# Kernel tuning notes

Measured on AMD Instinct MI355X. Metric: run time of the kernel, lower is better.

The kernel has to match this reference:

```python
import jax, jax.numpy as jnp
import numpy as np

BLOCK = 256
H, D = 16, 128          # num_attention_heads, head_dim
HID = 2048              # hidden_size (= H*D)
FFN = 2048              # intermediate_size
E, TOPK = 8, 2          # num_local_experts, num_experts_per_tok
EPS_LN = 1e-5           # rms_norm_eps for layer norms
EPS_ATTN = float(np.finfo(np.float32).eps)  # torch RMSNorm default eps


def rmsnorm(x, w, eps):
    v = jnp.mean(jnp.square(x), axis=-1, keepdims=True)
    return x * jax.lax.rsqrt(v + eps) * w


def lightning_attn(x, slope, qkv_w, gate_w, norm_w, out_w):
    # x: [B,N,HID]; slope: [H,1,1]
    B, N, _ = x.shape
    qkv = jax.nn.silu(x @ qkv_w.T).reshape(B, N, H, 3 * D)
    q, k, v = jnp.split(qkv, 3, axis=-1)
    q = q.transpose(0, 2, 1, 3)  # [B,H,N,D]
    k = k.transpose(0, 2, 1, 3)
    v = v.transpose(0, 2, 1, 3)

    NB = N // BLOCK
    ar = jnp.arange(BLOCK, dtype=jnp.float32) + 1.0
    q_decay = jnp.exp(-slope * ar[:, None])             # [H,BLOCK,1]
    k_decay = jnp.exp(-slope * (BLOCK - ar[:, None]))   # [H,BLOCK,1]
    idx = ar[:, None] - ar[None, :]                      # [BLOCK,BLOCK]
    diag_decay = jnp.exp(jnp.where(idx >= 0, -(slope * idx), -jnp.inf))  # [H,BLOCK,BLOCK]
    block_decay = jnp.exp(-slope * BLOCK)                # [H,1,1]

    qb = q.reshape(B, H, NB, BLOCK, D).transpose(2, 0, 1, 3, 4)  # [NB,B,H,BLOCK,D]
    kb = k.reshape(B, H, NB, BLOCK, D).transpose(2, 0, 1, 3, 4)
    vb = v.reshape(B, H, NB, BLOCK, D).transpose(2, 0, 1, 3, 4)

    def step(kv, blk):
        qi, ki, vi = blk                                   # [B,H,BLOCK,D]
        o_nd = jnp.einsum('bhmd,bhde->bhme', qi * q_decay, kv)
        qk = jnp.einsum('bhmd,bhnd->bhmn', qi, ki) * diag_decay[None]
        o_d = jnp.einsum('bhmn,bhne->bhme', qk, vi)
        kv = block_decay * kv + jnp.einsum('bhmd,bhme->bhde', ki * k_decay, vi)
        return kv, o_nd + o_d

    kv0 = jnp.zeros((B, H, D, D), jnp.float32)
    _, out = jax.lax.scan(step, kv0, (qb, kb, vb))         # out: [NB,B,H,BLOCK,D]
    out = out.transpose(1, 2, 0, 3, 4).reshape(B, H, N, D)
    out = out.transpose(0, 2, 1, 3).reshape(B, N, H * D)   # b h n d -> b n (h d)
    out = rmsnorm(out, norm_w, EPS_ATTN)
    out = jax.nn.sigmoid(x @ gate_w.T) * out
    return out @ out_w.T


def moe(x, router_w, w1, w2, w3):
    # x: [B,N,HID]
    B, N, _ = x.shape
    xt = x.reshape(B * N, HID)                             # [T,HID]
    T = B * N
    logits = xt @ router_w.T                               # [T,E]
    probs = jax.nn.softmax(logits.astype(jnp.float32), axis=-1)
    w, sel = jax.lax.top_k(probs, TOPK)                    # [T,TOPK]
    w = w / jnp.sum(w, axis=-1, keepdims=True)
    w = w.astype(xt.dtype)
    # dense combine weights [T,E] (top-k experts are distinct)
    cw = jnp.zeros((T, E), xt.dtype).at[jnp.arange(T)[:, None], sel].add(w)
    h1 = jax.nn.silu(jnp.einsum('td,efd->tef', xt, w1))    # [T,E,FFN]
    h3 = jnp.einsum('td,efd->tef', xt, w3)
    ye = jnp.einsum('tef,edf->ted', h1 * h3, w2)           # [T,E,HID]
    out = jnp.einsum('te,ted->td', cw, ye)
    return out.reshape(B, N, HID)


def setup_inputs() -> dict:
    key = jax.random.key(0)
    ks = jax.random.split(key, 12)
    s = 0.02
    B, N = 1, 1024
    x = jax.random.normal(ks[0], (B, N, HID), jnp.float32)
    # ALiBi-like positive per-head decay rates
    slope_rate = (1.0 / (2.0 ** (8.0 * (jnp.arange(H, dtype=jnp.float32) + 1) / H))).reshape(H, 1, 1)
    return {
        'x': x,
        'slope_rate': slope_rate,
        'ln1_w': jnp.ones((HID,), jnp.float32),
        'ln2_w': jnp.ones((HID,), jnp.float32),
        'qkv_w': jax.random.normal(ks[1], (3 * H * D, HID), jnp.float32) * s,
        'ogate_w': jax.random.normal(ks[2], (H * D, HID), jnp.float32) * s,
        'anorm_w': jnp.ones((H * D,), jnp.float32),
        'aout_w': jax.random.normal(ks[3], (HID, H * D), jnp.float32) * s,
        'router_w': jax.random.normal(ks[4], (E, HID), jnp.float32) * s,
        'w1': jax.random.normal(ks[5], (E, FFN, HID), jnp.float32) * s,
        'w2': jax.random.normal(ks[6], (E, HID, FFN), jnp.float32) * s,
        'w3': jax.random.normal(ks[7], (E, FFN, HID), jnp.float32) * s,
    }


def reference(x, slope_rate, ln1_w, ln2_w, qkv_w, ogate_w, anorm_w, aout_w, router_w, w1, w2, w3):
    # pre-norm residual decoder layer (alpha=beta=1, postnorm=False, no shared MoE)
    r = x
    h = rmsnorm(x, ln1_w, EPS_LN)
    h = r + lightning_attn(h, slope_rate, qkv_w, ogate_w, anorm_w, aout_w)
    r = h
    h2 = rmsnorm(h, ln2_w, EPS_LN)
    return r + moe(h2, router_w, w1, w2, w3)
```

## Files before the change

kernel.cpp:

```cpp
#include <hip/hip_runtime.h>
#include <math.h>

#define NTOK 1024
#define NHID 2048
#define NQKV 6144
#define NHEADS 16
#define DHEAD 128
#define ABLK 256
#define NEXPERT 8
#define NFFN 2048
#define EPS_LN 1e-5f
#define EPS_ATTN 1.1920929e-7f

typedef __bf16 bf8v __attribute__((ext_vector_type(8)));
typedef __bf16 bf4v __attribute__((ext_vector_type(4)));
typedef float f4v __attribute__((ext_vector_type(4)));

static __device__ __forceinline__ f4v mfma16(bf8v a, bf8v b, f4v c) {
  return __builtin_amdgcn_mfma_f32_16x16x32_bf16(a, b, c, 0, 0, 0);
}

static __device__ __forceinline__ void gl2lds16(const float* g, float* l) {
  __builtin_amdgcn_global_load_lds(
      (const __attribute__((address_space(1))) float*)g,
      (__attribute__((address_space(3))) float*)l, 16, 0, 0);
}

__global__ __launch_bounds__(256) void rms_kernel(const float* __restrict__ in,
                                                  const float* __restrict__ w,
                                                  float* __restrict__ out,
                                                  const float* __restrict__ gate,
                                                  float* __restrict__ copy_out,
                                                  float eps) {
  const int row = blockIdx.x, tid = threadIdx.x;
  const float* p = in + (size_t)row * NHID;
  float4 v0 = *(const float4*)(p + 4 * tid);
  float4 v1 = *(const float4*)(p + 1024 + 4 * tid);
  float ss = v0.x * v0.x + v0.y * v0.y + v0.z * v0.z + v0.w * v0.w
           + v1.x * v1.x + v1.y * v1.y + v1.z * v1.z + v1.w * v1.w;
  for (int off = 32; off > 0; off >>= 1) ss += __shfl_down(ss, off);
  __shared__ float red[4];
  const int wv = tid >> 6, ln = tid & 63;
  if (ln == 0) red[wv] = ss;
  __syncthreads();
  const float tot = red[0] + red[1] + red[2] + red[3];
  const float rinv = rsqrtf(tot * (1.f / NHID) + eps);
  float4 w0 = *(const float4*)(w + 4 * tid);
  float4 w1 = *(const float4*)(w + 1024 + 4 * tid);
  float4 o0, o1;
  o0.x = v0.x * rinv * w0.x; o0.y = v0.y * rinv * w0.y;
  o0.z = v0.z * rinv * w0.z; o0.w = v0.w * rinv * w0.w;
  o1.x = v1.x * rinv * w1.x; o1.y = v1.y * rinv * w1.y;
  o1.z = v1.z * rinv * w1.z; o1.w = v1.w * rinv * w1.w;
  if (gate) {
    const float* gp = gate + (size_t)row * NHID;
    float4 g0 = *(const float4*)(gp + 4 * tid);
    float4 g1 = *(const float4*)(gp + 1024 + 4 * tid);
    o0.x *= g0.x; o0.y *= g0.y; o0.z *= g0.z; o0.w *= g0.w;
    o1.x *= g1.x; o1.y *= g1.y; o1.z *= g1.z; o1.w *= g1.w;
  }
  *(float4*)(out + (size_t)row * NHID + 4 * tid) = o0;
  *(float4*)(out + (size_t)row * NHID + 1024 + 4 * tid) = o1;
  if (copy_out) {
    *(float4*)(copy_out + (size_t)row * NHID + 4 * tid) = v0;
    *(float4*)(copy_out + (size_t)row * NHID + 1024 + 4 * tid) = v1;
  }
}

enum { GM_QKV = 0, GM_GATE = 1, GM_AOUT = 2, GM_MOE1 = 3, GM_MOE3 = 4, GM_MOE2 = 5 };

struct GArgs {
  const float* A; const float* B; float* C;
  const float* res;
  float* q_s; float* k_s; float* v_s;
  const int* perm; const int* segoff; const float* pw;
  float* outp;
  int N, K;
};

template <int MODE>
__global__ __launch_bounds__(256, 3) void gemm_bt(GArgs g) {
  const int n0 = blockIdx.x * 64;
  const int m0 = blockIdx.y * 128;
  int segbase = 0, cnt = 0x40000000, e = 0;
  if constexpr (MODE >= GM_MOE1) {
    e = blockIdx.z;
    segbase = g.segoff[e];
    cnt = g.segoff[e + 1] - segbase;
    if (m0 >= cnt) return;
  }
  const float* Bp = g.B + (size_t)e * g.N * g.K + (size_t)n0 * g.K;
  __shared__ float As[2][128 * 32];
  __shared__ float Bs[2][64 * 32];
  const int tid = threadIdx.x;
  const int w = tid >> 6, lane = tid & 63;
  const int wm = (w >> 1) * 64, wn = (w & 1) * 32;
  const int lm = lane & 15, quad = lane >> 4;
  const int lr = lane >> 3;
  const int coff = ((lane & 7) ^ lr) * 4;
  const int K = g.K;

  const float* aptr[4];
  const float* bptr[2];
#pragma unroll
  for (int qi = 0; qi < 4; qi++) {
    const int r = (w * 4 + qi) * 8 + lr;
    const int m = m0 + r;
    long grow;
    if constexpr (MODE == GM_MOE1 || MODE == GM_MOE3) {
      int mm = m < cnt ? m : cnt - 1;
      grow = g.perm[segbase + mm];
    } else if constexpr (MODE == GM_MOE2) {
      grow = segbase + (m < cnt ? m : cnt - 1);
    } else {
      grow = m;
    }
    aptr[qi] = g.A + (size_t)grow * K + coff;
  }
#pragma unroll
  for (int qi = 0; qi < 2; qi++) {
    const int r = (w * 2 + qi) * 8 + lr;
    bptr[qi] = Bp + (size_t)r * K + coff;
  }

  const f4v fz = {0.f, 0.f, 0.f, 0.f};
  f4v acc[4][2];
#pragma unroll
  for (int i = 0; i < 4; i++) {
    acc[i][0] = fz; acc[i][1] = fz;
  }

  const int KT = K >> 5;
#pragma unroll
  for (int qi = 0; qi < 4; qi++) gl2lds16(aptr[qi], &As[0][(w * 4 + qi) * 256]);
#pragma unroll
  for (int qi = 0; qi < 2; qi++) gl2lds16(bptr[qi], &Bs[0][(w * 2 + qi) * 256]);
  asm volatile("s_waitcnt vmcnt(0)" ::: "memory");
  __builtin_amdgcn_s_barrier();

  for (int t = 0; t < KT; ++t) {
    const int cur = t & 1;
    if (t + 1 < KT) {
      const int k1 = (t + 1) << 5;
#pragma unroll
      for (int qi = 0; qi < 4; qi++)
        gl2lds16(aptr[qi] + k1, &As[cur ^ 1][(w * 4 + qi) * 256]);
#pragma unroll
      for (int qi = 0; qi < 2; qi++)
        gl2lds16(bptr[qi] + k1, &Bs[cur ^ 1][(w * 2 + qi) * 256]);
    }
    bf8v af[4], bfv[2];
    const int sw = lm & 7;
#pragma unroll
    for (int i = 0; i < 4; i++) {
      const int ra = wm + i * 16 + lm;
      const float4 x0 = *(const float4*)&As[cur][ra * 32 + (((quad * 2) ^ sw) << 2)];
      const float4 x1 = *(const float4*)&As[cur][ra * 32 + (((quad * 2 + 1) ^ sw) << 2)];
      bf8v t8;
      t8[0] = (__bf16)x0.x; t8[1] = (__bf16)x0.y; t8[2] = (__bf16)x0.z; t8[3] = (__bf16)x0.w;
      t8[4] = (__bf16)x1.x; t8[5] = (__bf16)x1.y; t8[6] = (__bf16)x1.z; t8[7] = (__bf16)x1.w;
      af[i] = t8;
    }
#pragma unroll
    for (int j = 0; j < 2; j++) {
      const int rb = wn + j * 16 + lm;
      const float4 x0 = *(const float4*)&Bs[cur][rb * 32 + (((quad * 2) ^ sw) << 2)];
      const float4 x1 = *(const float4*)&Bs[cur][rb * 32 + (((quad * 2 + 1) ^ sw) << 2)];
      bf8v t8;
      t8[0] = (__bf16)x0.x; t8[1] = (__bf16)x0.y; t8[2] = (__bf16)x0.z; t8[3] = (__bf16)x0.w;
      t8[4] = (__bf16)x1.x; t8[5] = (__bf16)x1.y; t8[6] = (__bf16)x1.z; t8[7] = (__bf16)x1.w;
      bfv[j] = t8;
    }
#pragma unroll
    for (int i = 0; i < 4; i++)
#pragma unroll
      for (int j = 0; j < 2; j++) acc[i][j] = mfma16(af[i], bfv[j], acc[i][j]);
    asm volatile("s_waitcnt vmcnt(0) lgkmcnt(0)" ::: "memory");
    __builtin_amdgcn_s_barrier();
  }

#pragma unroll
  for (int i = 0; i < 4; i++) {
#pragma unroll
    for (int r = 0; r < 4; r++) {
      const int m = m0 + wm + i * 16 + quad * 4 + r;
      int tok = 0;
      float wgt = 0.f;
      if constexpr (MODE == GM_MOE2) {
        if (m < cnt) { tok = g.perm[segbase + m]; wgt = g.pw[segbase + m]; }
      }
#pragma unroll
      for (int j = 0; j < 2; j++) {
        const int col = n0 + wn + j * 16 + lm;
        float v = acc[i][j][r];
        if constexpr (MODE == GM_QKV) {
          v = v / (1.f + expf(-v));
          int head = col / 384;
          int rem = col - head * 384;
          int which = rem >> 7;
          int d = rem & 127;
          float* dst = which == 0 ? g.q_s : (which == 1 ? g.k_s : g.v_s);
          dst[((size_t)head * NTOK + m) * DHEAD + d] = v;
        } else if constexpr (MODE == GM_GATE) {
          g.C[(size_t)m * g.N + col] = 1.f / (1.f + expf(-v));
        } else if constexpr (MODE == GM_AOUT) {
          g.C[(size_t)m * g.N + col] = v + g.res[(size_t)m * g.N + col];
        } else if constexpr (MODE == GM_MOE1) {
          if (m < cnt) g.C[(size_t)(segbase + m) * g.N + col] = v / (1.f + expf(-v));
        } else if constexpr (MODE == GM_MOE3) {
          if (m < cnt) {
            size_t ix = (size_t)(segbase + m) * g.N + col;
            g.C[ix] = v * g.res[ix];
          }
        } else if constexpr (MODE == GM_MOE2) {
          if (m < cnt) atomicAdd(&g.outp[(size_t)tok * NHID + col], wgt * v);
        }
      }
    }
  }
}

__global__ __launch_bounds__(512) void attn_pass1(const float* __restrict__ k_s,
                                                  const float* __restrict__ v_s,
                                                  const float* __restrict__ slope,
                                                  float* __restrict__ S) {
  const int h = blockIdx.x >> 2, b = blockIdx.x & 3;
  const float s = slope[h];
  __shared__ __bf16 kT[128][40] __attribute__((aligned(16)));
  __shared__ __bf16 vT[128][40] __attribute__((aligned(16)));
  const int tid = threadIdx.x, wave = tid >> 6, lane = tid & 63;
  const int lm = lane & 15, quad = lane >> 4;
  const float* kb = k_s + ((size_t)h * NTOK + b * ABLK) * DHEAD;
  const float* vb = v_s + ((size_t)h * NTOK + b * ABLK) * DHEAD;
  const int sd = tid & 127, sg = (tid >> 7) * 8;
  const f4v fz = {0.f, 0.f, 0.f, 0.f};
  f4v acc[8];
#pragma unroll
  for (int j = 0; j < 8; j++) acc[j] = fz;
  for (int ic = 0; ic < 8; ic++) {
    __syncthreads();
    bf8v kq, vq;
#pragma unroll
    for (int ii = 0; ii < 8; ii++) {
      int ig = ic * 32 + sg + ii;
      float kd = expf(-s * (float)(ABLK - 1 - ig));
      kq[ii] = (__bf16)(kb[(size_t)ig * DHEAD + sd] * kd);
      vq[ii] = (__bf16)(vb[(size_t)ig * DHEAD + sd]);
    }
    *(bf8v*)&kT[sd][sg] = kq;
    *(bf8v*)&vT[sd][sg] = vq;
    __syncthreads();
    bf8v a = *(const bf8v*)&kT[wave * 16 + lm][quad * 8];
#pragma unroll
    for (int j = 0; j < 8; j++) {
      bf8v bb = *(const bf8v*)&vT[j * 16 + lm][quad * 8];
      acc[j] = mfma16(a, bb, acc[j]);
    }
  }
  float* Sp = S + (size_t)(h * 4 + b) * (128 * 128);
#pragma unroll
  for (int j = 0; j < 8; j++)
#pragma unroll
    for (int r = 0; r < 4; r++)
      Sp[(size_t)(wave * 16 + quad * 4 + r) * 128 + j * 16 + lm] = acc[j][r];
}

__global__ __launch_bounds__(512) void attn_pass2(const float* __restrict__ q_s,
                                                  const float* __restrict__ k_s,
                                                  const float* __restrict__ v_s,
                                                  const float* __restrict__ slope,
                                                  const float* __restrict__ S,
                                                  float* __restrict__ attn_raw) {
  const int h = blockIdx.x >> 2, b = blockIdx.x & 3;
  const float s = slope[h];
  __shared__ __bf16 kvb[128][136] __attribute__((aligned(16)));
  __shared__ __bf16 vT[128][40] __attribute__((aligned(16)));
  __shared__ __bf16 ki[32][136] __attribute__((aligned(16)));
  __shared__ __bf16 qkb[256][40] __attribute__((aligned(16)));
  const int tid = threadIdx.x, w = tid >> 6, lane = tid & 63;
  const int lm = lane & 15, quad = lane >> 4;
  {
    const int sd = tid >> 2;
    const int e0 = (tid & 3) * 32;
    float vals[32];
#pragma unroll
    for (int u = 0; u < 32; u++) vals[u] = 0.f;
    for (int j = 0; j < b; j++) {
      float c = expf(-s * 256.f * (float)(b - 1 - j));
      const float* Sp = S + (size_t)(h * 4 + j) * (128 * 128) + (size_t)sd * 128 + e0;
#pragma unroll
      for (int u4 = 0; u4 < 8; u4++) {
        float4 sv = *(const float4*)(Sp + u4 * 4);
        vals[u4 * 4 + 0] += c * sv.x; vals[u4 * 4 + 1] += c * sv.y;
        vals[u4 * 4 + 2] += c * sv.z; vals[u4 * 4 + 3] += c * sv.w;
      }
    }
#pragma unroll
    for (int u = 0; u < 32; u++) kvb[e0 + u][sd] = (__bf16)vals[u];
  }
  __syncthreads();
  const float* qb = q_s + ((size_t)h * NTOK + b * ABLK) * DHEAD;
  const float* kb = k_s + ((size_t)h * NTOK + b * ABLK) * DHEAD;
  const float* vb = v_s + ((size_t)h * NTOK + b * ABLK) * DHEAD;
  bf8v aq[2][4];
#pragma unroll
  for (int mf = 0; mf < 2; mf++) {
    const int m = w * 32 + mf * 16 + lm;
#pragma unroll
    for (int kc = 0; kc < 4; kc++) {
      const float* pp = qb + (size_t)m * DHEAD + kc * 32 + quad * 8;
      float4 u0 = *(const float4*)pp;
      float4 u1 = *(const float4*)(pp + 4);
      bf8v t;
      t[0] = (__bf16)u0.x; t[1] = (__bf16)u0.y; t[2] = (__bf16)u0.z; t[3] = (__bf16)u0.w;
      t[4] = (__bf16)u1.x; t[5] = (__bf16)u1.y; t[6] = (__bf16)u1.z; t[7] = (__bf16)u1.w;
      aq[mf][kc] = t;
    }
  }
  const f4v fz = {0.f, 0.f, 0.f, 0.f};
  f4v accO[2][8];
#pragma unroll
  for (int mf = 0; mf < 2; mf++)
#pragma unroll
    for (int nf = 0; nf < 8; nf++) accO[mf][nf] = fz;
#pragma unroll
  for (int kc = 0; kc < 4; kc++) {
#pragma unroll
    for (int nf = 0; nf < 8; nf++) {
      bf8v bb = *(const bf8v*)&kvb[nf * 16 + lm][kc * 32 + quad * 8];
      accO[0][nf] = mfma16(aq[0][kc], bb, accO[0][nf]);
      accO[1][nf] = mfma16(aq[1][kc], bb, accO[1][nf]);
    }
  }
#pragma unroll
  for (int mf = 0; mf < 2; mf++) {
#pragma unroll
    for (int r = 0; r < 4; r++) {
      const int m = w * 32 + mf * 16 + quad * 4 + r;
      const float qd = expf(-s * (float)(m + 1));
#pragma unroll
      for (int nf = 0; nf < 8; nf++) accO[mf][nf][r] *= qd;
    }
  }
  for (int ic = 0; ic < 8; ic++) {
    __syncthreads();
    {
      const int si = tid >> 4, dc = (tid & 15) * 8;
      const float* pp = kb + (size_t)(ic * 32 + si) * DHEAD + dc;
      float4 u0 = *(const float4*)pp;
      float4 u1 = *(const float4*)(pp + 4);
      bf8v t;
      t[0] = (__bf16)u0.x; t[1] = (__bf16)u0.y; t[2] = (__bf16)u0.z; t[3] = (__bf16)u0.w;
      t[4] = (__bf16)u1.x; t[5] = (__bf16)u1.y; t[6] = (__bf16)u1.z; t[7] = (__bf16)u1.w;
      *(bf8v*)&ki[si][dc] = t;
    }
    {
      const int se = tid & 127, sg = (tid >> 7) * 8;
      bf8v t;
#pragma unroll
      for (int ii = 0; ii < 8; ii++)
        t[ii] = (__bf16)vb[(size_t)(ic * 32 + sg + ii) * DHEAD + se];
      *(bf8v*)&vT[se][sg] = t;
    }
    __syncthreads();
    f4v acc2[2][2];
    acc2[0][0] = fz; acc2[0][1] = fz; acc2[1][0] = fz; acc2[1][1] = fz;
#pragma unroll
    for (int kc = 0; kc < 4; kc++) {
#pragma unroll
      for (int f = 0; f < 2; f++) {
        bf8v bk = *(const bf8v*)&ki[f * 16 + lm][kc * 32 + quad * 8];
        acc2[0][f] = mfma16(aq[0][kc], bk, acc2[0][f]);
        acc2[1][f] = mfma16(aq[1][kc], bk, acc2[1][f]);
      }
    }
#pragma unroll
    for (int mf = 0; mf < 2; mf++) {
#pragma unroll
      for (int f = 0; f < 2; f++) {
#pragma unroll
        for (int r = 0; r < 4; r++) {
          const int m = w * 32 + mf * 16 + quad * 4 + r;
          const int i = ic * 32 + f * 16 + lm;
          float v = acc2[mf][f][r];
          v = (m >= i) ? v * expf(-s * (float)(m - i)) : 0.f;
          qkb[m][f * 16 + lm] = (__bf16)v;
        }
      }
    }
    __syncthreads();
#pragma unroll
    for (int mf = 0; mf < 2; mf++) {
      bf8v aqk = *(const bf8v*)&qkb[w * 32 + mf * 16 + lm][quad * 8];
#pragma unroll
      for (int nf = 0; nf < 8; nf++) {
        bf8v bv = *(const bf8v*)&vT[nf * 16 + lm][quad * 8];
        accO[mf][nf] = mfma16(aqk, bv, accO[mf][nf]);
      }
    }
  }
  float* op = attn_raw + (size_t)(b * ABLK) * NHID + h * DHEAD;
#pragma unroll
  for (int mf = 0; mf < 2; mf++)
#pragma unroll
    for (int r = 0; r < 4; r++) {
      const int m = w * 32 + mf * 16 + quad * 4 + r;
#pragma unroll
      for (int nf = 0; nf < 8; nf++)
        op[(size_t)m * NHID + nf * 16 + lm] = accO[mf][nf][r];
    }
}

__global__ __launch_bounds__(256) void router_kernel(const float* __restrict__ h2,
                                                     const float* __restrict__ rw,
                                                     int* __restrict__ eidx,
                                                     float* __restrict__ ew) {
  const int wave = threadIdx.x >> 6, lane = threadIdx.x & 63;
  const int t = blockIdx.x * 4 + wave;
  float a[8];
#pragma unroll
  for (int e = 0; e < 8; e++) a[e] = 0.f;
  for (int d = lane; d < NHID; d += 64) {
    float xv = h2[(size_t)t * NHID + d];
#pragma unroll
    for (int e = 0; e < 8; e++) a[e] += xv * rw[(size_t)e * NHID + d];
  }
#pragma unroll
  for (int e = 0; e < 8; e++)
    for (int off = 32; off > 0; off >>= 1) a[e] += __shfl_down(a[e], off);
  if (lane == 0) {
    int i1 = 0;
#pragma unroll
    for (int e = 1; e < 8; e++)
      if (a[e] > a[i1]) i1 = e;
    int i2 = i1 == 0 ? 1 : 0;
#pragma unroll
    for (int e = 0; e < 8; e++) {
      if (e == i1 || e == i2) continue;
      if (a[e] > a[i2]) i2 = e;
    }
    float be = expf(a[i2] - a[i1]);
    float w1 = 1.f / (1.f + be), w2 = be / (1.f + be);
    eidx[2 * t] = i1; eidx[2 * t + 1] = i2;
    ew[2 * t] = w1; ew[2 * t + 1] = w2;
  }
}

__global__ __launch_bounds__(256) void build_lists(const int* __restrict__ eidx,
                                                   const float* __restrict__ ew,
                                                   int* __restrict__ segoff,
                                                   int* __restrict__ perm,
                                                   float* __restrict__ pw) {
  __shared__ int cnt[8], cur[8], offs[9];
  const int tid = threadIdx.x;
  if (tid < 8) cnt[tid] = 0;
  __syncthreads();
  for (int t = tid; t < NTOK; t += 256) {
    atomicAdd(&cnt[eidx[2 * t]], 1);
    atomicAdd(&cnt[eidx[2 * t + 1]], 1);
  }
  __syncthreads();
  if (tid == 0) {
    int o = 0;
    for (int e = 0; e < 8; e++) { offs[e] = o; o += cnt[e]; }
    offs[8] = o;
    for (int e = 0; e < 9; e++) segoff[e] = offs[e];
  }
  __syncthreads();
  if (tid < 8) cur[tid] = offs[tid];
  __syncthreads();
  for (int t = tid; t < NTOK; t += 256) {
    for (int k = 0; k < 2; k++) {
      int e = eidx[2 * t + k];
      int pos = atomicAdd(&cur[e], 1);
      perm[pos] = t;
      pw[pos] = ew[2 * t + k];
    }
  }
}

extern "C" void kernel_launch(void* const* d_in, const int* in_sizes, int n_in,
                              void* d_out, int out_size, void* d_ws, size_t ws_size,
                              hipStream_t stream) {
  (void)in_sizes; (void)n_in; (void)out_size; (void)ws_size;
  const float* x        = (const float*)d_in[0];
  const float* slope    = (const float*)d_in[1];
  const float* ln1_w    = (const float*)d_in[2];
  const float* ln2_w    = (const float*)d_in[3];
  const float* qkv_w    = (const float*)d_in[4];
  const float* ogate_w  = (const float*)d_in[5];
  const float* anorm_w  = (const float*)d_in[6];
  const float* aout_w   = (const float*)d_in[7];
  const float* router_w = (const float*)d_in[8];
  const float* w1       = (const float*)d_in[9];
  const float* w2       = (const float*)d_in[10];
  const float* w3       = (const float*)d_in[11];
  float* out = (float*)d_out;
  float* ws  = (float*)d_ws;

  const size_t MW = (size_t)NTOK * NHID;
  float* a_ln     = ws;
  float* q_s      = ws + MW;
  float* k_s      = ws + 2 * MW;
  float* v_s      = ws + 3 * MW;
  float* Sbuf     = ws + 4 * MW;
  float* attn_raw = ws + 4 * MW + MW / 2;
  float* gatebuf  = ws + 5 * MW + MW / 2;
  float* t1       = ws + 4 * MW + MW / 2;
  float* rbase    = ws + 6 * MW + MW / 2;
  int*   eidx   = (int*)rbase;
  float* ew     = rbase + 2048;
  int*   segoff = (int*)(rbase + 4096);
  int*   perm   = (int*)(rbase + 4112);
  float* pw     = rbase + 6160;
  float* h_res = k_s;
  float* h2    = v_s;
  float* ag    = a_ln;

  rms_kernel<<<dim3(NTOK), dim3(256), 0, stream>>>(x, ln1_w, a_ln, nullptr, nullptr, EPS_LN);
  {
    GArgs g{}; g.A = a_ln; g.B = qkv_w; g.q_s = q_s; g.k_s = k_s; g.v_s = v_s;
    g.N = NQKV; g.K = NHID;
    gemm_bt<GM_QKV><<<dim3(NQKV / 64, NTOK / 128), dim3(256), 0, stream>>>(g);
  }
  attn_pass1<<<dim3(64), dim3(512), 0, stream>>>(k_s, v_s, slope, Sbuf);
  attn_pass2<<<dim3(64), dim3(512), 0, stream>>>(q_s, k_s, v_s, slope, Sbuf, attn_raw);
  {
    GArgs g{}; g.A = a_ln; g.B = ogate_w; g.C = gatebuf; g.N = NHID; g.K = NHID;
    gemm_bt<GM_GATE><<<dim3(32, 8), dim3(256), 0, stream>>>(g);
  }
  rms_kernel<<<dim3(NTOK), dim3(256), 0, stream>>>(attn_raw, anorm_w, ag, gatebuf, nullptr, EPS_ATTN);
  {
    GArgs g{}; g.A = ag; g.B = aout_w; g.C = h_res; g.res = x; g.N = NHID; g.K = NHID;
    gemm_bt<GM_AOUT><<<dim3(32, 8), dim3(256), 0, stream>>>(g);
  }
  rms_kernel<<<dim3(NTOK), dim3(256), 0, stream>>>(h_res, ln2_w, h2, nullptr, out, EPS_LN);
  router_kernel<<<dim3(NTOK / 4), dim3(256), 0, stream>>>(h2, router_w, eidx, ew);
  build_lists<<<dim3(1), dim3(256), 0, stream>>>(eidx, ew, segoff, perm, pw);
  {
    GArgs g{}; g.A = h2; g.B = w1; g.C = t1; g.perm = perm; g.segoff = segoff;
    g.N = NFFN; g.K = NHID;
    gemm_bt<GM_MOE1><<<dim3(32, 16, 8), dim3(256), 0, stream>>>(g);
  }
  {
    GArgs g{}; g.A = h2; g.B = w3; g.C = t1; g.res = t1; g.perm = perm; g.segoff = segoff;
    g.N = NFFN; g.K = NHID;
    gemm_bt<GM_MOE3><<<dim3(32, 16, 8), dim3(256), 0, stream>>>(g);
  }
  {
    GArgs g{}; g.A = t1; g.B = w2; g.outp = out; g.perm = perm; g.segoff = segoff; g.pw = pw;
    g.N = NHID; g.K = NFFN;
    gemm_bt<GM_MOE2><<<dim3(32, 16, 8), dim3(256), 0, stream>>>(g);
  }
}
```

Before: 874.8 us.

## Store activations in bf16 and triple-buffer GEMM LDS staging

RMSNorm outputs, the q/k/v buffers and the MoE intermediate are now written in bf16 instead of fp32. This halves activation traffic and lets the GEMM A-tile and the attention kernels load bf16 directly, with no per-tile conversion. The GEMM main loop moves from a double-buffered to a three-stage LDS pipeline with partial vmcnt waits, so loads run two tiles ahead. The cost is extra rounding of activations and intermediates (t1 is rounded twice) and more shared memory per block, which may reduce occupancy.

```diff
diff --git a/kernel.cpp b/kernel.cpp
--- a/kernel.cpp
+++ b/kernel.cpp
@@ -20,17 +20,18 @@
   return __builtin_amdgcn_mfma_f32_16x16x32_bf16(a, b, c, 0, 0, 0);
 }
 
-static __device__ __forceinline__ void gl2lds16(const float* g, float* l) {
+static __device__ __forceinline__ void gl2lds16(const void* g, void* l) {
   __builtin_amdgcn_global_load_lds(
-      (const __attribute__((address_space(1))) float*)g,
-      (__attribute__((address_space(3))) float*)l, 16, 0, 0);
+      (const __attribute__((address_space(1))) unsigned int*)g,
+      (__attribute__((address_space(3))) unsigned int*)l, 16, 0, 0);
 }
 
 __global__ __launch_bounds__(256) void rms_kernel(const float* __restrict__ in,
                                                   const float* __restrict__ w,
-                                                  float* __restrict__ out,
+                                                  __bf16* __restrict__ out_bf,
                                                   const float* __restrict__ gate,
                                                   float* __restrict__ copy_out,
+                                                  float* __restrict__ out_f32,
                                                   float eps) {
   const int row = blockIdx.x, tid = threadIdx.x;
   const float* p = in + (size_t)row * NHID;
@@ -59,8 +60,15 @@
     o0.x *= g0.x; o0.y *= g0.y; o0.z *= g0.z; o0.w *= g0.w;
     o1.x *= g1.x; o1.y *= g1.y; o1.z *= g1.z; o1.w *= g1.w;
   }
-  *(float4*)(out + (size_t)row * NHID + 4 * tid) = o0;
-  *(float4*)(out + (size_t)row * NHID + 1024 + 4 * tid) = o1;
+  bf4v b0, b1;
+  b0[0] = (__bf16)o0.x; b0[1] = (__bf16)o0.y; b0[2] = (__bf16)o0.z; b0[3] = (__bf16)o0.w;
+  b1[0] = (__bf16)o1.x; b1[1] = (__bf16)o1.y; b1[2] = (__bf16)o1.z; b1[3] = (__bf16)o1.w;
+  *(bf4v*)(out_bf + (size_t)row * NHID + 4 * tid) = b0;
+  *(bf4v*)(out_bf + (size_t)row * NHID + 1024 + 4 * tid) = b1;
+  if (out_f32) {
+    *(float4*)(out_f32 + (size_t)row * NHID + 4 * tid) = o0;
+    *(float4*)(out_f32 + (size_t)row * NHID + 1024 + 4 * tid) = o1;
+  }
   if (copy_out) {
     *(float4*)(copy_out + (size_t)row * NHID + 4 * tid) = v0;
     *(float4*)(copy_out + (size_t)row * NHID + 1024 + 4 * tid) = v1;
@@ -70,9 +78,9 @@
 enum { GM_QKV = 0, GM_GATE = 1, GM_AOUT = 2, GM_MOE1 = 3, GM_MOE3 = 4, GM_MOE2 = 5 };
 
 struct GArgs {
-  const float* A; const float* B; float* C;
+  const __bf16* A; const float* B; void* C;
   const float* res;
-  float* q_s; float* k_s; float* v_s;
+  __bf16* q_s; __bf16* k_s; __bf16* v_s;
   const int* perm; const int* segoff; const float* pw;
   float* outp;
   int N, K;
@@ -90,21 +98,18 @@
     if (m0 >= cnt) return;
   }
   const float* Bp = g.B + (size_t)e * g.N * g.K + (size_t)n0 * g.K;
-  __shared__ float As[2][128 * 32];
-  __shared__ float Bs[2][64 * 32];
+  __shared__ __bf16 As[3][128 * 32] __attribute__((aligned(16)));
+  __shared__ float Bs[3][64 * 32] __attribute__((aligned(16)));
   const int tid = threadIdx.x;
   const int w = tid >> 6, lane = tid & 63;
   const int wm = (w >> 1) * 64, wn = (w & 1) * 32;
   const int lm = lane & 15, quad = lane >> 4;
-  const int lr = lane >> 3;
-  const int coff = ((lane & 7) ^ lr) * 4;
   const int K = g.K;
 
-  const float* aptr[4];
-  const float* bptr[2];
-#pragma unroll
-  for (int qi = 0; qi < 4; qi++) {
-    const int r = (w * 4 + qi) * 8 + lr;
+  const __bf16* aptr[2];
+#pragma unroll
+  for (int qi = 0; qi < 2; qi++) {
+    const int r = w * 32 + qi * 16 + (lane >> 2);
     const int m = m0 + r;
     long grow;
     if constexpr (MODE == GM_MOE1 || MODE == GM_MOE3) {
@@ -115,12 +120,18 @@
     } else {
       grow = m;
     }
-    aptr[qi] = g.A + (size_t)grow * K + coff;
-  }
-#pragma unroll
-  for (int qi = 0; qi < 2; qi++) {
-    const int r = (w * 2 + qi) * 8 + lr;
-    bptr[qi] = Bp + (size_t)r * K + coff;
+    const int gc = (lane & 3) ^ (r & 3);
+    aptr[qi] = g.A + (size_t)grow * K + gc * 8;
+  }
+  const float* bptr[2];
+  {
+    const int lr = lane >> 3;
+    const int coff = ((lane & 7) ^ lr) * 4;
+#pragma unroll
+    for (int qi = 0; qi < 2; qi++) {
+      const int r = (w * 2 + qi) * 8 + lr;
+      bptr[qi] = Bp + (size_t)r * K + coff;
+    }
   }
 
   const f4v fz = {0.f, 0.f, 0.f, 0.f};
@@ -131,41 +142,44 @@
   }
 
   const int KT = K >> 5;
-#pragma unroll
-  for (int qi = 0; qi < 4; qi++) gl2lds16(aptr[qi], &As[0][(w * 4 + qi) * 256]);
-#pragma unroll
-  for (int qi = 0; qi < 2; qi++) gl2lds16(bptr[qi], &Bs[0][(w * 2 + qi) * 256]);
-  asm volatile("s_waitcnt vmcnt(0)" ::: "memory");
-  __builtin_amdgcn_s_barrier();
-
+
+#define STAGE(tt, bb)                                      \
+  do {                                                     \
+    const int kk_ = (tt) << 5;                             \
+    gl2lds16(aptr[0] + kk_, &As[bb][(w * 32) * 32]);       \
+    gl2lds16(aptr[1] + kk_, &As[bb][(w * 32 + 16) * 32]);  \
+    gl2lds16(bptr[0] + kk_, &Bs[bb][(w * 16) * 32]);       \
+    gl2lds16(bptr[1] + kk_, &Bs[bb][(w * 16 + 8) * 32]);   \
+  } while (0)
+
+  STAGE(0, 0);
+  STAGE(1, 1);
+
+  const int swa = lm & 3;
+  const int swb = lm & 7;
   for (int t = 0; t < KT; ++t) {
-    const int cur = t & 1;
+    const int cur = t % 3;
     if (t + 1 < KT) {
-      const int k1 = (t + 1) << 5;
-#pragma unroll
-      for (int qi = 0; qi < 4; qi++)
-        gl2lds16(aptr[qi] + k1, &As[cur ^ 1][(w * 4 + qi) * 256]);
-#pragma unroll
-      for (int qi = 0; qi < 2; qi++)
-        gl2lds16(bptr[qi] + k1, &Bs[cur ^ 1][(w * 2 + qi) * 256]);
+      asm volatile("s_waitcnt vmcnt(4)" ::: "memory");
+    } else {
+      asm volatile("s_waitcnt vmcnt(0)" ::: "memory");
+    }
+    __builtin_amdgcn_s_barrier();
+    if (t + 2 < KT) {
+      const int nb = (t + 2) % 3;
+      STAGE(t + 2, nb);
     }
     bf8v af[4], bfv[2];
-    const int sw = lm & 7;
 #pragma unroll
     for (int i = 0; i < 4; i++) {
       const int ra = wm + i * 16 + lm;
-      const float4 x0 = *(const float4*)&As[cur][ra * 32 + (((quad * 2) ^ sw) << 2)];
-      const float4 x1 = *(const float4*)&As[cur][ra * 32 + (((quad * 2 + 1) ^ sw) << 2)];
-      bf8v t8;
-      t8[0] = (__bf16)x0.x; t8[1] = (__bf16)x0.y; t8[2] = (__bf16)x0.z; t8[3] = (__bf16)x0.w;
-      t8[4] = (__bf16)x1.x; t8[5] = (__bf16)x1.y; t8[6] = (__bf16)x1.z; t8[7] = (__bf16)x1.w;
-      af[i] = t8;
+      af[i] = *(const bf8v*)&As[cur][ra * 32 + ((quad ^ swa) << 3)];
     }
 #pragma unroll
     for (int j = 0; j < 2; j++) {
       const int rb = wn + j * 16 + lm;
-      const float4 x0 = *(const float4*)&Bs[cur][rb * 32 + (((quad * 2) ^ sw) << 2)];
-      const float4 x1 = *(const float4*)&Bs[cur][rb * 32 + (((quad * 2 + 1) ^ sw) << 2)];
+      const float4 x0 = *(const float4*)&Bs[cur][rb * 32 + (((quad * 2) ^ swb) << 2)];
+      const float4 x1 = *(const float4*)&Bs[cur][rb * 32 + (((quad * 2 + 1) ^ swb) << 2)];
       bf8v t8;
       t8[0] = (__bf16)x0.x; t8[1] = (__bf16)x0.y; t8[2] = (__bf16)x0.z; t8[3] = (__bf16)x0.w;
       t8[4] = (__bf16)x1.x; t8[5] = (__bf16)x1.y; t8[6] = (__bf16)x1.z; t8[7] = (__bf16)x1.w;
@@ -175,9 +189,8 @@
     for (int i = 0; i < 4; i++)
 #pragma unroll
       for (int j = 0; j < 2; j++) acc[i][j] = mfma16(af[i], bfv[j], acc[i][j]);
-    asm volatile("s_waitcnt vmcnt(0) lgkmcnt(0)" ::: "memory");
-    __builtin_amdgcn_s_barrier();
-  }
+  }
+#undef STAGE
 
 #pragma unroll
   for (int i = 0; i < 4; i++) {
@@ -199,18 +212,20 @@
           int rem = col - head * 384;
           int which = rem >> 7;
           int d = rem & 127;
-          float* dst = which == 0 ? g.q_s : (which == 1 ? g.k_s : g.v_s);
-          dst[((size_t)head * NTOK + m) * DHEAD + d] = v;
+          __bf16* dst = which == 0 ? g.q_s : (which == 1 ? g.k_s : g.v_s);
+          dst[((size_t)head * NTOK + m) * DHEAD + d] = (__bf16)v;
         } else if constexpr (MODE == GM_GATE) {
-          g.C[(size_t)m * g.N + col] = 1.f / (1.f + expf(-v));
+          ((float*)g.C)[(size_t)m * g.N + col] = 1.f / (1.f + expf(-v));
         } else if constexpr (MODE == GM_AOUT) {
-          g.C[(size_t)m * g.N + col] = v + g.res[(size_t)m * g.N + col];
+          ((float*)g.C)[(size_t)m * g.N + col] = v + g.res[(size_t)m * g.N + col];
         } else if constexpr (MODE == GM_MOE1) {
-          if (m < cnt) g.C[(size_t)(segbase + m) * g.N + col] = v / (1.f + expf(-v));
+          if (m < cnt)
+            ((__bf16*)g.C)[(size_t)(segbase + m) * g.N + col] = (__bf16)(v / (1.f + expf(-v)));
         } else if constexpr (MODE == GM_MOE3) {
           if (m < cnt) {
             size_t ix = (size_t)(segbase + m) * g.N + col;
-            g.C[ix] = v * g.res[ix];
+            __bf16* tc = (__bf16*)g.C;
+            tc[ix] = (__bf16)(v * (float)tc[ix]);
           }
         } else if constexpr (MODE == GM_MOE2) {
           if (m < cnt) atomicAdd(&g.outp[(size_t)tok * NHID + col], wgt * v);
@@ -220,8 +235,8 @@
   }
 }
 
-__global__ __launch_bounds__(512) void attn_pass1(const float* __restrict__ k_s,
-                                                  const float* __restrict__ v_s,
+__global__ __launch_bounds__(512) void attn_pass1(const __bf16* __restrict__ k_s,
+                                                  const __bf16* __restrict__ v_s,
                                                   const float* __restrict__ slope,
                                                   float* __restrict__ S) {
   const int h = blockIdx.x >> 2, b = blockIdx.x & 3;
@@ -230,8 +245,8 @@
   __shared__ __bf16 vT[128][40] __attribute__((aligned(16)));
   const int tid = threadIdx.x, wave = tid >> 6, lane = tid & 63;
   const int lm = lane & 15, quad = lane >> 4;
-  const float* kb = k_s + ((size_t)h * NTOK + b * ABLK) * DHEAD;
-  const float* vb = v_s + ((size_t)h * NTOK + b * ABLK) * DHEAD;
+  const __bf16* kb = k_s + ((size_t)h * NTOK + b * ABLK) * DHEAD;
+  const __bf16* vb = v_s + ((size_t)h * NTOK + b * ABLK) * DHEAD;
   const int sd = tid & 127, sg = (tid >> 7) * 8;
   const f4v fz = {0.f, 0.f, 0.f, 0.f};
   f4v acc[8];
@@ -244,8 +259,8 @@
     for (int ii = 0; ii < 8; ii++) {
       int ig = ic * 32 + sg + ii;
       float kd = expf(-s * (float)(ABLK - 1 - ig));
-      kq[ii] = (__bf16)(kb[(size_t)ig * DHEAD + sd] * kd);
-      vq[ii] = (__bf16)(vb[(size_t)ig * DHEAD + sd]);
+      kq[ii] = (__bf16)((float)kb[(size_t)ig * DHEAD + sd] * kd);
+      vq[ii] = vb[(size_t)ig * DHEAD + sd];
     }
     *(bf8v*)&kT[sd][sg] = kq;
     *(bf8v*)&vT[sd][sg] = vq;
@@ -265,9 +280,9 @@
       Sp[(size_t)(wave * 16 + quad * 4 + r) * 128 + j * 16 + lm] = acc[j][r];
 }
 
-__global__ __launch_bounds__(512) void attn_pass2(const float* __restrict__ q_s,
-                                                  const float* __restrict__ k_s,
-                                                  const float* __restrict__ v_s,
+__global__ __launch_bounds__(512) void attn_pass2(const __bf16* __restrict__ q_s,
+                                                  const __bf16* __restrict__ k_s,
+                                                  const __bf16* __restrict__ v_s,
                                                   const float* __restrict__ slope,
                                                   const float* __restrict__ S,
                                                   float* __restrict__ attn_raw) {
@@ -299,23 +314,16 @@
     for (int u = 0; u < 32; u++) kvb[e0 + u][sd] = (__bf16)vals[u];
   }
   __syncthreads();
-  const float* qb = q_s + ((size_t)h * NTOK + b * ABLK) * DHEAD;
-  const float* kb = k_s + ((size_t)h * NTOK + b * ABLK) * DHEAD;
-  const float* vb = v_s + ((size_t)h * NTOK + b * ABLK) * DHEAD;
+  const __bf16* qb = q_s + ((size_t)h * NTOK + b * ABLK) * DHEAD;
+  const __bf16* kb = k_s + ((size_t)h * NTOK + b * ABLK) * DHEAD;
+  const __bf16* vb = v_s + ((size_t)h * NTOK + b * ABLK) * DHEAD;
   bf8v aq[2][4];
 #pragma unroll
   for (int mf = 0; mf < 2; mf++) {
     const int m = w * 32 + mf * 16 + lm;
 #pragma unroll
-    for (int kc = 0; kc < 4; kc++) {
-      const float* pp = qb + (size_t)m * DHEAD + kc * 32 + quad * 8;
-      float4 u0 = *(const float4*)pp;
-      float4 u1 = *(const float4*)(pp + 4);
-      bf8v t;
-      t[0] = (__bf16)u0.x; t[1] = (__bf16)u0.y; t[2] = (__bf16)u0.z; t[3] = (__bf16)u0.w;
-      t[4] = (__bf16)u1.x; t[5] = (__bf16)u1.y; t[6] = (__bf16)u1.z; t[7] = (__bf16)u1.w;
-      aq[mf][kc] = t;
-    }
+    for (int kc = 0; kc < 4; kc++)
+      aq[mf][kc] = *(const bf8v*)(qb + (size_t)m * DHEAD + kc * 32 + quad * 8);
   }
   const f4v fz = {0.f, 0.f, 0.f, 0.f};
   f4v accO[2][8];
@@ -346,20 +354,14 @@
     __syncthreads();
     {
       const int si = tid >> 4, dc = (tid & 15) * 8;
-      const float* pp = kb + (size_t)(ic * 32 + si) * DHEAD + dc;
-      float4 u0 = *(const float4*)pp;
-      float4 u1 = *(const float4*)(pp + 4);
-      bf8v t;
-      t[0] = (__bf16)u0.x; t[1] = (__bf16)u0.y; t[2] = (__bf16)u0.z; t[3] = (__bf16)u0.w;
-      t[4] = (__bf16)u1.x; t[5] = (__bf16)u1.y; t[6] = (__bf16)u1.z; t[7] = (__bf16)u1.w;
-      *(bf8v*)&ki[si][dc] = t;
+      *(bf8v*)&ki[si][dc] = *(const bf8v*)(kb + (size_t)(ic * 32 + si) * DHEAD + dc);
     }
     {
       const int se = tid & 127, sg = (tid >> 7) * 8;
       bf8v t;
 #pragma unroll
       for (int ii = 0; ii < 8; ii++)
-        t[ii] = (__bf16)vb[(size_t)(ic * 32 + sg + ii) * DHEAD + se];
+        t[ii] = vb[(size_t)(ic * 32 + sg + ii) * DHEAD + se];
       *(bf8v*)&vT[se][sg] = t;
     }
     __syncthreads();
@@ -499,25 +501,26 @@
   float* ws  = (float*)d_ws;
 
   const size_t MW = (size_t)NTOK * NHID;
-  float* a_ln     = ws;
-  float* q_s      = ws + MW;
-  float* k_s      = ws + 2 * MW;
-  float* v_s      = ws + 3 * MW;
-  float* Sbuf     = ws + 4 * MW;
+  __bf16* a_ln   = (__bf16*)ws;
+  __bf16* q_s    = (__bf16*)(ws + MW);
+  __bf16* k_s    = (__bf16*)(ws + 2 * MW);
+  __bf16* v_s    = (__bf16*)(ws + 3 * MW);
+  float* Sbuf    = ws + 4 * MW;
   float* attn_raw = ws + 4 * MW + MW / 2;
   float* gatebuf  = ws + 5 * MW + MW / 2;
-  float* t1       = ws + 4 * MW + MW / 2;
-  float* rbase    = ws + 6 * MW + MW / 2;
+  __bf16* t1     = (__bf16*)attn_raw;
+  float* h2f     = gatebuf;
+  float* rbase   = ws + 6 * MW + MW / 2;
   int*   eidx   = (int*)rbase;
   float* ew     = rbase + 2048;
   int*   segoff = (int*)(rbase + 4096);
   int*   perm   = (int*)(rbase + 4112);
   float* pw     = rbase + 6160;
-  float* h_res = k_s;
-  float* h2    = v_s;
-  float* ag    = a_ln;
-
-  rms_kernel<<<dim3(NTOK), dim3(256), 0, stream>>>(x, ln1_w, a_ln, nullptr, nullptr, EPS_LN);
+  float* h_res  = ws + 2 * MW;
+  __bf16* h2    = v_s;
+  __bf16* ag    = a_ln;
+
+  rms_kernel<<<dim3(NTOK), dim3(256), 0, stream>>>(x, ln1_w, a_ln, nullptr, nullptr, nullptr, EPS_LN);
   {
     GArgs g{}; g.A = a_ln; g.B = qkv_w; g.q_s = q_s; g.k_s = k_s; g.v_s = v_s;
     g.N = NQKV; g.K = NHID;
@@ -529,13 +532,13 @@
     GArgs g{}; g.A = a_ln; g.B = ogate_w; g.C = gatebuf; g.N = NHID; g.K = NHID;
     gemm_bt<GM_GATE><<<dim3(32, 8), dim3(256), 0, stream>>>(g);
   }
-  rms_kernel<<<dim3(NTOK), dim3(256), 0, stream>>>(attn_raw, anorm_w, ag, gatebuf, nullptr, EPS_ATTN);
+  rms_kernel<<<dim3(NTOK), dim3(256), 0, stream>>>(attn_raw, anorm_w, ag, gatebuf, nullptr, nullptr, EPS_ATTN);
   {
     GArgs g{}; g.A = ag; g.B = aout_w; g.C = h_res; g.res = x; g.N = NHID; g.K = NHID;
     gemm_bt<GM_AOUT><<<dim3(32, 8), dim3(256), 0, stream>>>(g);
   }
-  rms_kernel<<<dim3(NTOK), dim3(256), 0, stream>>>(h_res, ln2_w, h2, nullptr, out, EPS_LN);
-  router_kernel<<<dim3(NTOK / 4), dim3(256), 0, stream>>>(h2, router_w, eidx, ew);
+  rms_kernel<<<dim3(NTOK), dim3(256), 0, stream>>>(h_res, ln2_w, h2, nullptr, out, h2f, EPS_LN);
+  router_kernel<<<dim3(NTOK / 4), dim3(256), 0, stream>>>(h2f, router_w, eidx, ew);
   build_lists<<<dim3(1), dim3(256), 0, stream>>>(eidx, ew, segoff, perm, pw);
   {
     GArgs g{}; g.A = h2; g.B = w1; g.C = t1; g.perm = perm; g.segoff = segoff;
@@ -543,7 +546,7 @@
     gemm_bt<GM_MOE1><<<dim3(32, 16, 8), dim3(256), 0, stream>>>(g);
   }
   {
-    GArgs g{}; g.A = h2; g.B = w3; g.C = t1; g.res = t1; g.perm = perm; g.segoff = segoff;
+    GArgs g{}; g.A = h2; g.B = w3; g.C = t1; g.perm = perm; g.segoff = segoff;
     g.N = NFFN; g.K = NHID;
     gemm_bt<GM_MOE3><<<dim3(32, 16, 8), dim3(256), 0, stream>>>(g);
   }
```

Result: faster. 824.7 us (-5.7%).
